# Optimization experiments

Hardware: AMD Instinct MI355X
Metric: run time of the kernel (lower is better)

## Reference

```python
import jax, jax.numpy as jnp
import numpy as np

CONF_THRESHOLD = 0.7

def setup_inputs() -> dict:
    key = jax.random.key(0)
    ks = jax.random.split(key, 8)
    B, T, D, H, GH = 16384, 48, 32, 1024, 128
    s = lambda fan: 1.0 / np.sqrt(fan)
    return {
        "x":   jax.random.normal(ks[0], (B, T, D), jnp.float32),
        "gW1": jax.random.normal(ks[1], (D, GH), jnp.float32) * s(D),
        "gb1": jnp.zeros((GH,), jnp.float32),
        "gW2": jax.random.normal(ks[2], (GH, 2), jnp.float32) * s(GH),
        "gb2": jnp.zeros((2,), jnp.float32),
        "nW1": jax.random.normal(ks[3], (T * D, H), jnp.float32) * s(T * D),
        "nb1": jnp.zeros((H,), jnp.float32),
        "nW2": jax.random.normal(ks[4], (H, 2), jnp.float32) * s(H),
        "nb2": jnp.zeros((2,), jnp.float32),
        "aW1": jax.random.normal(ks[5], (T * D, H), jnp.float32) * s(T * D),
        "ab1": jnp.zeros((H,), jnp.float32),
        "aW2": jax.random.normal(ks[6], (H, 2), jnp.float32) * s(H),
        "ab2": jnp.zeros((2,), jnp.float32),
    }

def _gate(x, gW1, gb1, gW2, gb2):
    # mean-pool over time, 2-layer MLP, softmax -> [B, 2] class probs
    h = jax.nn.relu(jnp.mean(x, axis=1) @ gW1 + gb1)
    return jax.nn.softmax(h @ gW2 + gb2, axis=-1)

def _expert(x_flat, W1, b1, W2, b2):
    return jax.nn.relu(x_flat @ W1 + b1) @ W2 + b2

def reference(x, gW1, gb1, gW2, gb2, nW1, nb1, nW2, nb2, aW1, ab1, aW2, ab2):
    B = x.shape[0]
    gate_outputs = _gate(x, gW1, gb1, gW2, gb2)          # [B, 2]
    gate_probs = jnp.max(gate_outputs, axis=1)           # [B]
    gate_decisions = jnp.argmax(gate_outputs, axis=1)    # [B] in {0,1}

    # adaptive routing: low-confidence samples fall back to the normal expert
    high_conf = gate_probs >= CONF_THRESHOLD
    abnormal_mask = high_conf & (gate_decisions == 1)
    # normal_mask = (high_conf & dec==0) | ~high_conf  == ~abnormal_mask (partition)

    x_flat = x.reshape(B, -1)
    normal_out = _expert(x_flat, nW1, nb1, nW2, nb2)     # [B, 2]
    abnormal_out = _expert(x_flat, aW1, ab1, aW2, ab2)   # [B, 2]
    outputs = jnp.where(abnormal_mask[:, None], abnormal_out, normal_out)
    return outputs, gate_decisions, gate_probs
```

## Files before the change

kernel.cpp:

```cpp
#include <hip/hip_runtime.h>

#define TDIM 48
#define DDIM 32
#define KDIM 1536
#define HDIM 1024
#define GHID 128

typedef unsigned short u16;
typedef __bf16 bf16x8 __attribute__((ext_vector_type(8)));
typedef float  f32x4  __attribute__((ext_vector_type(4)));

typedef const void __attribute__((address_space(1))) gvoid;
typedef void       __attribute__((address_space(3))) lvoid;

__device__ __forceinline__ void gld_lds16(const void* g, void* l) {
    __builtin_amdgcn_global_load_lds((gvoid*)g, (lvoid*)l, 16, 0, 0);
}

__device__ __forceinline__ u16 f2bf(float f) {
    union { float f; unsigned u; } v; v.f = f;
    return (u16)((v.u + 0x7fffu + ((v.u >> 16) & 1u)) >> 16);
}

__global__ __launch_bounds__(256) void gate_kernel(
    const float* __restrict__ x,
    const float* __restrict__ gW1, const float* __restrict__ gb1,
    const float* __restrict__ gW2, const float* __restrict__ gb2,
    u16* __restrict__ Xbf, int* __restrict__ route, int* __restrict__ cnt,
    float* __restrict__ out, float* __restrict__ outDec, float* __restrict__ outProb)
{
    const int wave = threadIdx.x >> 6;
    const int lane = threadIdx.x & 63;
    const int b    = blockIdx.x * 4 + wave;
    if (blockIdx.x == 0 && threadIdx.x < 2) cnt[threadIdx.x] = 0;

    const float* xr = x + (size_t)b * KDIM;
    u16* xo = Xbf + (size_t)b * KDIM;

    double a0 = 0, a1 = 0, a2 = 0, a3 = 0;
#pragma unroll
    for (int i = 0; i < 6; ++i) {
        const int idx = i * 256 + lane * 4;
        float4 v = *(const float4*)(xr + idx);
        ushort4 o;
        o.x = f2bf(v.x); o.y = f2bf(v.y); o.z = f2bf(v.z); o.w = f2bf(v.w);
        *(ushort4*)(xo + idx) = o;
        a0 += v.x; a1 += v.y; a2 += v.z; a3 += v.w;
    }
#pragma unroll
    for (int m = 8; m <= 32; m <<= 1) {
        a0 += __shfl_xor(a0, m); a1 += __shfl_xor(a1, m);
        a2 += __shfl_xor(a2, m); a3 += __shfl_xor(a3, m);
    }
    __shared__ double xm[4][DDIM];
    if (lane < 8) {
        xm[wave][4 * lane + 0] = a0 / 48.0; xm[wave][4 * lane + 1] = a1 / 48.0;
        xm[wave][4 * lane + 2] = a2 / 48.0; xm[wave][4 * lane + 3] = a3 / 48.0;
    }
    __builtin_amdgcn_wave_barrier();
    __builtin_amdgcn_s_waitcnt(0);
    __threadfence_block();

    double h0 = (double)gb1[lane], h1 = (double)gb1[lane + 64];
#pragma unroll
    for (int d = 0; d < DDIM; ++d) {
        const double xv = xm[wave][d];
        h0 += xv * (double)gW1[d * GHID + lane];
        h1 += xv * (double)gW1[d * GHID + 64 + lane];
    }
    h0 = h0 > 0.0 ? h0 : 0.0;
    h1 = h1 > 0.0 ? h1 : 0.0;
    double z0 = h0 * (double)gW2[lane * 2 + 0] + h1 * (double)gW2[(lane + 64) * 2 + 0];
    double z1 = h0 * (double)gW2[lane * 2 + 1] + h1 * (double)gW2[(lane + 64) * 2 + 1];
#pragma unroll
    for (int m = 1; m <= 32; m <<= 1) {
        z0 += __shfl_xor(z0, m);
        z1 += __shfl_xor(z1, m);
    }
    if (lane == 0) {
        z0 += (double)gb2[0]; z1 += (double)gb2[1];
        const int dec = (z1 > z0) ? 1 : 0;
        const double mz = z0 > z1 ? z0 : z1;
        const double e0 = exp(z0 - mz), e1 = exp(z1 - mz);
        const double p = (e0 > e1 ? e0 : e1) / (e0 + e1);
        const float pf = (float)p;
        outDec[b]  = (float)dec;
        outProb[b] = pf;
        out[2 * b + 0] = 0.f;
        out[2 * b + 1] = 0.f;
        const int high = ((double)pf >= 0.7) ? 1 : 0;
        route[b] = (high && dec) ? 1 : 0;
    }
}

__global__ __launch_bounds__(256) void transpose_cast(
    const float* __restrict__ nW1, const float* __restrict__ aW1,
    u16* __restrict__ W1t)
{
    __shared__ float tile[32][33];
    const int e  = blockIdx.z;
    const float* W = e ? aW1 : nW1;
    u16* Wt = W1t + (size_t)e * HDIM * KDIM;
    const int bx = blockIdx.x;
    const int by = blockIdx.y;
    const int tx = threadIdx.x;
    const int ty = threadIdx.y;
#pragma unroll
    for (int r = 0; r < 32; r += 8)
        tile[ty + r][tx] = W[(size_t)(by * 32 + ty + r) * HDIM + bx * 32 + tx];
    __syncthreads();
#pragma unroll
    for (int r = 0; r < 32; r += 8)
        Wt[(size_t)(bx * 32 + ty + r) * KDIM + by * 32 + tx] = f2bf(tile[tx][ty + r]);
}

__global__ __launch_bounds__(256) void compact_kernel(
    const int* __restrict__ route, int* __restrict__ perm, int* __restrict__ cnt,
    int Bn)
{
    const int b    = blockIdx.x * 256 + threadIdx.x;
    const int lane = threadIdx.x & 63;
    const int active = (b < Bn);
    const int e = active ? route[b] : 0;
    const unsigned long long m1 = __ballot(active && e == 1);
    const unsigned long long m0 = __ballot(active && e == 0);
    const unsigned long long below = (lane == 63) ? ~0ull >> 1 : ((1ull << lane) - 1);
    int base0 = 0, base1 = 0;
    if (lane == 0) {
        if (m0) base0 = atomicAdd(&cnt[0], (int)__popcll(m0));
        if (m1) base1 = atomicAdd(&cnt[1], (int)__popcll(m1));
    }
    base0 = __shfl(base0, 0);
    base1 = __shfl(base1, 0);
    if (active) {
        const int pos = e ? base1 + (int)__popcll(m1 & below)
                          : base0 + (int)__popcll(m0 & below);
        perm[e * Bn + pos] = b;
    }
}

__global__ __launch_bounds__(256, 2) void expert_gemm(
    const u16* __restrict__ Xbf, const u16* __restrict__ W1t,
    const float* __restrict__ nb1, const float* __restrict__ nW2,
    const float* __restrict__ nb2,
    const float* __restrict__ ab1, const float* __restrict__ aW2,
    const float* __restrict__ ab2,
    const int* __restrict__ perm, const int* __restrict__ cnt,
    float* __restrict__ out, int Bn, int mBlocks)
{
    __shared__ __align__(16) u16 Alds[128 * 64];
    __shared__ __align__(16) u16 Blds[128 * 64];
    __shared__ int   permLds[128];
    __shared__ float w2Lds[128 * 2];
    __shared__ float b1Lds[128];

    const int tid = threadIdx.x;
    const int f    = (int)blockIdx.x;
    const int g4   = f >> 6;
    const int nIdx = (f >> 3) & 7;
    const int mGlb = g4 * 8 + (f & 7);
    const int e  = mGlb >= mBlocks;
    const int mb = mGlb - (e ? mBlocks : 0);
    const int cntE = cnt[e];
    const int start = mb * 128;
    if (start >= cntE) return;
    const int valid = min(128, cntE - start);

    const int n0 = nIdx * 128;
    const u16*  W1e = W1t + (size_t)e * HDIM * KDIM;
    const float* b1 = e ? ab1 : nb1;
    const float* w2 = e ? aW2 : nW2;
    const float* b2 = e ? ab2 : nb2;

    if (tid < 128) permLds[tid] = perm[e * Bn + min(start + tid, cntE - 1)];
    if (tid >= 128) {
        const int j = tid - 128;
        b1Lds[j]        = b1[n0 + j];
        w2Lds[j * 2 + 0] = w2[(n0 + j) * 2 + 0];
        w2Lds[j * 2 + 1] = w2[(n0 + j) * 2 + 1];
    }
    __syncthreads();

    const int rbase = tid >> 3;
    const int cg    = (tid & 7) ^ (rbase & 7);
    const u16* gA[4]; const u16* gB[4];
#pragma unroll
    for (int j = 0; j < 4; ++j) {
        gA[j] = Xbf + (size_t)permLds[rbase + 32 * j] * KDIM + cg * 8;
        gB[j] = W1e + (size_t)(n0 + rbase + 32 * j) * KDIM + cg * 8;
    }
    u16* la = (u16*)Alds + tid * 8;
    u16* lb = (u16*)Blds + tid * 8;

    const int wave = tid >> 6;
    const int lane = tid & 63;
    const int wm   = (wave & 1) * 64;
    const int wn   = (wave >> 1) * 64;
    const int l15  = lane & 15;
    const int quad = lane >> 4;

    f32x4 acc[4][4];
#pragma unroll
    for (int i = 0; i < 4; ++i)
#pragma unroll
        for (int j = 0; j < 4; ++j) acc[i][j] = (f32x4)0.f;

    for (int k0 = 0; k0 < KDIM; k0 += 64) {
#pragma unroll
        for (int j = 0; j < 4; ++j)
            gld_lds16(gA[j] + k0, la + j * 2048);
#pragma unroll
        for (int j = 0; j < 4; ++j)
            gld_lds16(gB[j] + k0, lb + j * 2048);
        __syncthreads();

#pragma unroll
        for (int t = 0; t < 2; ++t) {
            bf16x8 af[4], bfv[4];
#pragma unroll
            for (int mi = 0; mi < 4; ++mi) {
                const int r = wm + mi * 16 + l15;
                const int p = (t * 4 + quad) ^ (r & 7);
                af[mi] = *reinterpret_cast<const bf16x8*>(&Alds[r * 64 + p * 8]);
            }
#pragma unroll
            for (int ni = 0; ni < 4; ++ni) {
                const int r = wn + ni * 16 + l15;
                const int p = (t * 4 + quad) ^ (r & 7);
                bfv[ni] = *reinterpret_cast<const bf16x8*>(&Blds[r * 64 + p * 8]);
            }
#pragma unroll
            for (int mi = 0; mi < 4; ++mi)
#pragma unroll
                for (int ni = 0; ni < 4; ++ni)
                    acc[mi][ni] = __builtin_amdgcn_mfma_f32_16x16x32_bf16(af[mi], bfv[ni], acc[mi][ni], 0, 0, 0);
        }
        __syncthreads();
    }

    const float b2_0 = (n0 == 0) ? b2[0] : 0.f;
    const float b2_1 = (n0 == 0) ? b2[1] : 0.f;
#pragma unroll
    for (int mi = 0; mi < 4; ++mi) {
        float p0[4] = {0.f, 0.f, 0.f, 0.f};
        float p1[4] = {0.f, 0.f, 0.f, 0.f};
#pragma unroll
        for (int ni = 0; ni < 4; ++ni) {
            const int col = wn + ni * 16 + l15;
            const float w20 = w2Lds[col * 2 + 0];
            const float w21 = w2Lds[col * 2 + 1];
            const float bb  = b1Lds[col];
#pragma unroll
            for (int r = 0; r < 4; ++r) {
                float h = acc[mi][ni][r] + bb;
                h = fmaxf(h, 0.f);
                p0[r] += h * w20;
                p1[r] += h * w21;
            }
        }
#pragma unroll
        for (int m = 1; m <= 8; m <<= 1) {
#pragma unroll
            for (int r = 0; r < 4; ++r) {
                p0[r] += __shfl_xor(p0[r], m);
                p1[r] += __shfl_xor(p1[r], m);
            }
        }
        if (l15 < 4) {
            const int r = l15;
            const int lrow = wm + mi * 16 + quad * 4 + r;
            if (lrow < valid) {
                const int srow = permLds[lrow];
                atomicAdd(&out[srow * 2 + 0], p0[r] + b2_0);
                atomicAdd(&out[srow * 2 + 1], p1[r] + b2_1);
            }
        }
    }
}

extern "C" void kernel_launch(void* const* d_in, const int* in_sizes, int n_in,
                              void* d_out, int out_size, void* d_ws, size_t ws_size,
                              hipStream_t stream) {
    const float* x   = (const float*)d_in[0];
    const float* gW1 = (const float*)d_in[1];
    const float* gb1 = (const float*)d_in[2];
    const float* gW2 = (const float*)d_in[3];
    const float* gb2 = (const float*)d_in[4];
    const float* nW1 = (const float*)d_in[5];
    const float* nb1 = (const float*)d_in[6];
    const float* nW2 = (const float*)d_in[7];
    const float* nb2 = (const float*)d_in[8];
    const float* aW1 = (const float*)d_in[9];
    const float* ab1 = (const float*)d_in[10];
    const float* aW2 = (const float*)d_in[11];
    const float* ab2 = (const float*)d_in[12];

    float* out = (float*)d_out;
    const int Bn = in_sizes[0] / KDIM;

    char* ws = (char*)d_ws;
    size_t off = 0;
    u16* Xbf = (u16*)(ws + off); off += (size_t)Bn * KDIM * sizeof(u16);
    u16* W1t = (u16*)(ws + off); off += (size_t)2 * HDIM * KDIM * sizeof(u16);
    int* perm = (int*)(ws + off); off += (size_t)2 * Bn * sizeof(int);
    int* cnt  = (int*)(ws + off); off += 2 * sizeof(int);
    int* route = (int*)(ws + off); off += (size_t)Bn * sizeof(int);

    gate_kernel<<<Bn / 4, 256, 0, stream>>>(x, gW1, gb1, gW2, gb2,
                                            Xbf, route, cnt,
                                            out, out + 2 * Bn, out + 3 * Bn);

    transpose_cast<<<dim3(HDIM / 32, KDIM / 32, 2), dim3(32, 8), 0, stream>>>(nW1, aW1, W1t);

    compact_kernel<<<(Bn + 255) / 256, 256, 0, stream>>>(route, perm, cnt, Bn);

    const int mBlocks = (Bn + 127) / 128;
    expert_gemm<<<8 * 2 * mBlocks, 256, 0, stream>>>(
        Xbf, W1t, nb1, nW2, nb2, ab1, aW2, ab2, perm, cnt, out, Bn, mBlocks);
}
```

Baseline: 247.6 us.

## Fuse compaction with weight transpose, use nontemporal x loads, raise GEMM occupancy

Merges the routing-compaction kernel and the weight transpose/cast kernel into one launch, with block index ranges selecting which job a block does. This removes one kernel launch and its serialization. It also switches the gate kernel's input reads to nontemporal loads, and raises the expert GEMM launch-bounds occupancy hint from 2 to 4 waves per SIMD, which may force register spilling. The compaction branch hardcodes 64 blocks, which assumes Bn <= 16384.

```diff
diff --git a/kernel.cpp b/kernel.cpp
--- a/kernel.cpp
+++ b/kernel.cpp
@@ -41,11 +41,11 @@
 #pragma unroll
     for (int i = 0; i < 6; ++i) {
         const int idx = i * 256 + lane * 4;
-        float4 v = *(const float4*)(xr + idx);
+        f32x4 v = __builtin_nontemporal_load((const f32x4*)(xr + idx));
         ushort4 o;
-        o.x = f2bf(v.x); o.y = f2bf(v.y); o.z = f2bf(v.z); o.w = f2bf(v.w);
+        o.x = f2bf(v[0]); o.y = f2bf(v[1]); o.z = f2bf(v[2]); o.w = f2bf(v[3]);
         *(ushort4*)(xo + idx) = o;
-        a0 += v.x; a1 += v.y; a2 += v.z; a3 += v.w;
+        a0 += v[0]; a1 += v[1]; a2 += v[2]; a3 += v[3];
     }
 #pragma unroll
     for (int m = 8; m <= 32; m <<= 1) {
@@ -93,53 +93,57 @@
     }
 }
 
-__global__ __launch_bounds__(256) void transpose_cast(
+__global__ __launch_bounds__(256) void compact_transpose(
+    const int* __restrict__ route, int* __restrict__ perm, int* __restrict__ cnt,
+    int Bn,
     const float* __restrict__ nW1, const float* __restrict__ aW1,
     u16* __restrict__ W1t)
 {
     __shared__ float tile[32][33];
-    const int e  = blockIdx.z;
-    const float* W = e ? aW1 : nW1;
-    u16* Wt = W1t + (size_t)e * HDIM * KDIM;
-    const int bx = blockIdx.x;
-    const int by = blockIdx.y;
-    const int tx = threadIdx.x;
-    const int ty = threadIdx.y;
-#pragma unroll
-    for (int r = 0; r < 32; r += 8)
-        tile[ty + r][tx] = W[(size_t)(by * 32 + ty + r) * HDIM + bx * 32 + tx];
-    __syncthreads();
-#pragma unroll
-    for (int r = 0; r < 32; r += 8)
-        Wt[(size_t)(bx * 32 + ty + r) * KDIM + by * 32 + tx] = f2bf(tile[tx][ty + r]);
-}
-
-__global__ __launch_bounds__(256) void compact_kernel(
-    const int* __restrict__ route, int* __restrict__ perm, int* __restrict__ cnt,
-    int Bn)
-{
-    const int b    = blockIdx.x * 256 + threadIdx.x;
-    const int lane = threadIdx.x & 63;
-    const int active = (b < Bn);
-    const int e = active ? route[b] : 0;
-    const unsigned long long m1 = __ballot(active && e == 1);
-    const unsigned long long m0 = __ballot(active && e == 0);
-    const unsigned long long below = (lane == 63) ? ~0ull >> 1 : ((1ull << lane) - 1);
-    int base0 = 0, base1 = 0;
-    if (lane == 0) {
-        if (m0) base0 = atomicAdd(&cnt[0], (int)__popcll(m0));
-        if (m1) base1 = atomicAdd(&cnt[1], (int)__popcll(m1));
-    }
-    base0 = __shfl(base0, 0);
-    base1 = __shfl(base1, 0);
-    if (active) {
-        const int pos = e ? base1 + (int)__popcll(m1 & below)
-                          : base0 + (int)__popcll(m0 & below);
-        perm[e * Bn + pos] = b;
-    }
-}
-
-__global__ __launch_bounds__(256, 2) void expert_gemm(
+    const int blk = (int)blockIdx.x;
+    const int tid = threadIdx.x;
+
+    if (blk < 64) {
+        const int b    = blk * 256 + tid;
+        const int lane = tid & 63;
+        const int active = (b < Bn);
+        const int e = active ? route[b] : 0;
+        const unsigned long long m1 = __ballot(active && e == 1);
+        const unsigned long long m0 = __ballot(active && e == 0);
+        const unsigned long long below = (lane == 63) ? ~0ull >> 1 : ((1ull << lane) - 1);
+        int base0 = 0, base1 = 0;
+        if (lane == 0) {
+            if (m0) base0 = atomicAdd(&cnt[0], (int)__popcll(m0));
+            if (m1) base1 = atomicAdd(&cnt[1], (int)__popcll(m1));
+        }
+        base0 = __shfl(base0, 0);
+        base1 = __shfl(base1, 0);
+        if (active) {
+            const int pos = e ? base1 + (int)__popcll(m1 & below)
+                              : base0 + (int)__popcll(m0 & below);
+            perm[e * Bn + pos] = b;
+        }
+    } else {
+        int t = blk - 64;
+        const int e = t >= (32 * 48);
+        t -= e ? (32 * 48) : 0;
+        const int bx = t & 31;
+        const int by = t >> 5;
+        const float* W = e ? aW1 : nW1;
+        u16* Wt = W1t + (size_t)e * HDIM * KDIM;
+        const int tx = tid & 31;
+        const int ty = tid >> 5;
+#pragma unroll
+        for (int r = 0; r < 32; r += 8)
+            tile[ty + r][tx] = W[(size_t)(by * 32 + ty + r) * HDIM + bx * 32 + tx];
+        __syncthreads();
+#pragma unroll
+        for (int r = 0; r < 32; r += 8)
+            Wt[(size_t)(bx * 32 + ty + r) * KDIM + by * 32 + tx] = f2bf(tile[tx][ty + r]);
+    }
+}
+
+__global__ __launch_bounds__(256, 4) void expert_gemm(
     const u16* __restrict__ Xbf, const u16* __restrict__ W1t,
     const float* __restrict__ nb1, const float* __restrict__ nW2,
     const float* __restrict__ nb2,
@@ -310,9 +314,8 @@
                                             Xbf, route, cnt,
                                             out, out + 2 * Bn, out + 3 * Bn);
 
-    transpose_cast<<<dim3(HDIM / 32, KDIM / 32, 2), dim3(32, 8), 0, stream>>>(nW1, aW1, W1t);
-
-    compact_kernel<<<(Bn + 255) / 256, 256, 0, stream>>>(route, perm, cnt, Bn);
+    compact_transpose<<<64 + 2 * (HDIM / 32) * (KDIM / 32), 256, 0, stream>>>(
+        route, perm, cnt, Bn, nW1, aW1, W1t);
 
     const int mBlocks = (Bn + 127) / 128;
     expert_gemm<<<8 * 2 * mBlocks, 256, 0, stream>>>(
```

Measured after the change: 237.0 us, median of 2. 4.3% less time.
